# Kernel optimization log

Measured on AMD Instinct MI355X. Metric: run time of the kernel, lower is better.

The kernel has to match this reference:

```python
import jax, jax.numpy as jnp
import numpy as np

B, D, H = 256, 512, 256
K = 5
MARGIN = 1.0
TAU = 1.0
LAM_C = 0.01
LAM_E = 0.1
BETA = 0.1
LN_EPS = 1e-5


def _layernorm(x, g, b):
    mu = jnp.mean(x, axis=-1, keepdims=True)
    var = jnp.var(x, axis=-1, keepdims=True)
    return (x - mu) * jax.lax.rsqrt(var + LN_EPS) * g + b


def setup_inputs() -> dict:
    key = jax.random.key(0)
    ks = jax.random.split(key, 16)
    s = 0.02
    inp = {
        "outputs": jax.random.normal(ks[0], (B, 3, 64, 64), jnp.float32),
        "images": jax.random.normal(ks[1], (B, 3, 64, 64), jnp.float32),
        "f_orig": jax.random.normal(ks[2], (B, D), jnp.float32),
        "f_recon": jax.random.normal(ks[3], (B, D), jnp.float32),
        "cf1": jax.random.normal(ks[4], (B, 256, 8, 8), jnp.float32),
        "cf2": jax.random.normal(ks[5], (B, 512, 4, 4), jnp.float32),
        # EnergyNet encoder params
        "W1": jax.random.normal(ks[6], (D, H), jnp.float32) * s,
        "b1": jnp.zeros((H,), jnp.float32),
        "g1": jnp.ones((H,), jnp.float32),
        "be1": jnp.zeros((H,), jnp.float32),
        "W2": jax.random.normal(ks[7], (H, H), jnp.float32) * s,
        "b2": jnp.zeros((H,), jnp.float32),
        # EnergyNet interaction params
        "W3": jax.random.normal(ks[8], (3 * H, H), jnp.float32) * s,
        "b3": jnp.zeros((H,), jnp.float32),
        "g3": jnp.ones((H,), jnp.float32),
        "be3": jnp.zeros((H,), jnp.float32),
        "W4": jax.random.normal(ks[9], (H, H // 2), jnp.float32) * s,
        "b4": jnp.zeros((H // 2,), jnp.float32),
        "W5": jax.random.normal(ks[10], (H // 2, 1), jnp.float32) * s,
        "b5": jnp.zeros((1,), jnp.float32),
    }
    return inp


def _encoder(x, W1, b1, g1, be1, W2, b2):
    h = _layernorm(x @ W1 + b1, g1, be1)
    return jax.nn.relu(h) @ W2 + b2


def _energy_matrix(f1, f2, W1, b1, g1, be1, W2, b2, W3, b3, g3, be3, W4, b4, W5, b5):
    e1 = _encoder(f1, W1, b1, g1, be1, W2, b2)  # [B,H]
    e2 = _encoder(f2, W1, b1, g1, be1, W2, b2)  # [B,H]
    e1b = jnp.broadcast_to(e1[:, None, :], (B, B, H))
    e2b = jnp.broadcast_to(e2[None, :, :], (B, B, H))
    combined = jnp.concatenate([e1b, e2b, e1b * e2b], axis=-1)  # [B,B,3H]
    h = jax.nn.relu(_layernorm(combined @ W3 + b3, g3, be3))
    h = jax.nn.relu(h @ W4 + b4)
    return (h @ W5 + b5)[..., 0]  # [B,B]


def _topk_neighbors(f, k):
    fn = f / (jnp.linalg.norm(f, axis=1, keepdims=True))
    sim = fn @ fn.T
    sim = jnp.where(jnp.eye(f.shape[0], dtype=bool), -jnp.inf, sim)
    _, idx = jax.lax.top_k(sim, k)  # [B,k]
    onehot = jnp.zeros((f.shape[0], f.shape[0]), jnp.float32)
    rows = jnp.arange(f.shape[0])[:, None]
    return onehot.at[rows, idx].set(1.0)


def _entropy(x):
    xn = (x - x.min()) / (x.max() - x.min() + 1e-8)
    # torch.histc(bins=256, min=0, max=1): values at max go to last bin
    idx = jnp.clip(jnp.floor(xn.reshape(-1) * 256.0).astype(jnp.int32), 0, 255)
    hist = jnp.bincount(idx, length=256).astype(jnp.float32)
    p = hist / hist.sum()
    return -jnp.sum(p * jnp.log2(p + 1e-8))


def reference(outputs, images, f_orig, f_recon, cf1, cf2,
              W1, b1, g1, be1, W2, b2, W3, b3, g3, be3, W4, b4, W5, b5):
    # reconstruction loss
    recon = jnp.mean((outputs - images) ** 2)

    # energy margin loss
    E = _energy_matrix(f_orig, f_recon, W1, b1, g1, be1, W2, b2,
                       W3, b3, g3, be3, W4, b4, W5, b5)
    pos = jnp.diag(E)[:, None]
    losses = jax.nn.relu(MARGIN + E - pos)
    neg_mask = ~jnp.eye(B, dtype=bool)
    standard_loss = jnp.sum(losses * neg_mask) / (B * (B - 1))

    k = min(K, B - 1)
    on = _topk_neighbors(f_orig, k)
    rn = _topk_neighbors(f_recon, k)
    inter = jnp.sum(on * rn, axis=1)
    union = jnp.sum(jnp.clip(on + rn, 0.0, 1.0), axis=1)
    jaccard = inter / (union + 1e-8)
    neighbor_loss = 1.0 - jnp.mean(jaccard)
    energy_loss = standard_loss + 0.3 * neighbor_loss

    # compression loss over the dict of compressed features {cf1, cf2}
    sp = 0.5 * (jnp.mean(jnp.abs(cf1)) + jnp.mean(jnp.abs(cf2)))
    en = 0.5 * (_entropy(cf1) + _entropy(cf2))
    compress = sp + BETA * en

    total = recon + LAM_C * compress + LAM_E * energy_loss
    return (total, recon, energy_loss, compress)
```

## Files before the change

### kernel.cpp

```cpp
#include <hip/hip_runtime.h>
#include <math.h>

typedef __attribute__((ext_vector_type(8))) short short8;
typedef __attribute__((ext_vector_type(4))) float f32x4;


__device__ __forceinline__ float wave_sum(float v) {
#pragma unroll
    for (int o = 32; o > 0; o >>= 1) v += __shfl_down(v, o);
    return v;
}

__device__ __forceinline__ float block_sum256(float v, float* red) {
    v = wave_sum(v);
    int t = threadIdx.x;
    if ((t & 63) == 0) red[t >> 6] = v;
    __syncthreads();
    float r = red[0] + red[1] + red[2] + red[3];
    __syncthreads();
    return r;
}

__device__ __forceinline__ unsigned fenc(float f) {
    unsigned u = __float_as_uint(f);
    return (u & 0x80000000u) ? ~u : (u | 0x80000000u);
}
__device__ __forceinline__ float fdec(unsigned u) {
    return (u & 0x80000000u) ? __uint_as_float(u & 0x7fffffffu) : __uint_as_float(~u);
}

__device__ __forceinline__ ushort f2bf(float f) {
    unsigned u = __float_as_uint(f);
    unsigned r = (u + 0x7fffu + ((u >> 16) & 1u)) >> 16;
    return (ushort)r;
}


__global__ void init_kernel(float* wsf, unsigned* wsu, int* wsi) {
    int t = threadIdx.x;
    if (t < 7) wsf[t] = 0.f;
    if (t == 7 || t == 9) wsu[t] = 0xFFFFFFFFu;
    if (t == 8 || t == 10) wsu[t] = 0u;
    wsi[16 + t] = 0;
    wsi[272 + t] = 0;
}

__global__ __launch_bounds__(256) void stats_kernel(
    const float4* __restrict__ o, const float4* __restrict__ im,
    const float4* __restrict__ cf1, const float4* __restrict__ cf2,
    const float4* __restrict__ fo, const float4* __restrict__ fr,
    float* wsf, unsigned* wsu, float* rnorm) {
    __shared__ float red[4];
    __shared__ float rmn[4], rmx[4];
    int b = blockIdx.x, t = threadIdx.x;
    if (b < 512) {
        float s = 0.f;
        for (int i = b * 256 + t; i < 786432; i += 512 * 256) {
            float4 a = o[i], c = im[i];
            float dx = a.x - c.x, dy = a.y - c.y, dz = a.z - c.z, dw = a.w - c.w;
            s += dx * dx + dy * dy + dz * dz + dw * dw;
        }
        float tot = block_sum256(s, red);
        if (t == 0) atomicAdd(wsf + 0, tot);
    } else if (b < 1536) {
        int which = (b < 1024) ? 0 : 1;
        const float4* x = which ? cf2 : cf1;
        int n4 = which ? 524288 : 1048576;
        int b0 = which ? 1024 : 512;
        float s = 0.f, mn = INFINITY, mx = -INFINITY;
        for (int i = (b - b0) * 256 + t; i < n4; i += 512 * 256) {
            float4 a = x[i];
            s += fabsf(a.x) + fabsf(a.y) + fabsf(a.z) + fabsf(a.w);
            mn = fminf(mn, fminf(fminf(a.x, a.y), fminf(a.z, a.w)));
            mx = fmaxf(mx, fmaxf(fmaxf(a.x, a.y), fmaxf(a.z, a.w)));
        }
        float tot = block_sum256(s, red);
#pragma unroll
        for (int off = 32; off > 0; off >>= 1) {
            mn = fminf(mn, __shfl_down(mn, off));
            mx = fmaxf(mx, __shfl_down(mx, off));
        }
        if ((t & 63) == 0) { rmn[t >> 6] = mn; rmx[t >> 6] = mx; }
        __syncthreads();
        if (t == 0) {
            atomicAdd(wsf + 1 + which, tot);
            float m1 = fminf(fminf(rmn[0], rmn[1]), fminf(rmn[2], rmn[3]));
            float m2 = fmaxf(fmaxf(rmx[0], rmx[1]), fmaxf(rmx[2], rmx[3]));
            atomicMin(wsu + 7 + which * 2, fenc(m1));
            atomicMax(wsu + 8 + which * 2, fenc(m2));
        }
    } else {
        int r = b - 1536;
        const float4* f = (r < 256) ? (fo + (size_t)r * 128) : (fr + (size_t)(r - 256) * 128);
        float s = 0.f;
        if (t < 128) {
            float4 a = f[t];
            s = a.x * a.x + a.y * a.y + a.z * a.z + a.w * a.w;
        }
        float tot = block_sum256(s, red);
        if (t == 0) rnorm[r] = 1.0f / sqrtf(tot);
    }
}

__global__ __launch_bounds__(256) void hist_kernel(const float4* __restrict__ cf1,
                                                   const float4* __restrict__ cf2,
                                                   const unsigned* wsu, int* wsi) {
    __shared__ int hl[256];
    int b = blockIdx.x, t = threadIdx.x;
    hl[t] = 0;
    __syncthreads();
    int which = (b < 512) ? 0 : 1;
    const float4* x = which ? cf2 : cf1;
    int n4 = which ? 524288 : 1048576;
    int b0 = which ? 512 : 0;
    int* hist = wsi + (which ? 272 : 16);
    float mn = fdec(wsu[7 + which * 2]), mx = fdec(wsu[8 + which * 2]);
    float inv = 256.f / (mx - mn + 1e-8f);
    for (int i = (b - b0) * 256 + t; i < n4; i += 512 * 256) {
        float4 a = x[i];
        int b0i = min(max((int)floorf((a.x - mn) * inv), 0), 255);
        int b1i = min(max((int)floorf((a.y - mn) * inv), 0), 255);
        int b2i = min(max((int)floorf((a.z - mn) * inv), 0), 255);
        int b3i = min(max((int)floorf((a.w - mn) * inv), 0), 255);
        atomicAdd(&hl[b0i], 1);
        atomicAdd(&hl[b1i], 1);
        atomicAdd(&hl[b2i], 1);
        atomicAdd(&hl[b3i], 1);
    }
    __syncthreads();
    if (hl[t]) atomicAdd(&hist[t], hl[t]);
}

__global__ __launch_bounds__(256) void transpose_kernel(const float* __restrict__ fo,
                                                        const float* __restrict__ fr,
                                                        const float* __restrict__ rnorm,
                                                        float* __restrict__ fnT) {
    int b = blockIdx.x;
    int pass = b >> 6;
    int kt = (b >> 2) & 15;
    int jt = b & 3;
    int k0 = kt * 32, j0 = jt * 64;
    const float* f = pass ? fr : fo;
    const float* rn = rnorm + pass * 256;
    __shared__ float tile[64][33];
    int t = threadIdx.x;
    int cl = t & 31, rl = t >> 5;
#pragma unroll
    for (int r = 0; r < 8; ++r) {
        int row = j0 + rl + r * 8;
        tile[rl + r * 8][cl] = f[(size_t)row * 512 + k0 + cl] * rn[row];
    }
    __syncthreads();
    int jl = t & 63, kq = t >> 6;
    float* dst = fnT + (size_t)pass * 131072;
#pragma unroll
    for (int c = 0; c < 8; ++c) {
        int kl = kq * 8 + c;
        dst[(size_t)(k0 + kl) * 256 + j0 + jl] = tile[jl][kl];
    }
}

__global__ __launch_bounds__(256) void simtop_kernel(const float* __restrict__ fo,
                                                     const float* __restrict__ fr,
                                                     const float* __restrict__ rnorm,
                                                     const float* __restrict__ fnT,
                                                     int* __restrict__ top5) {
    int b = blockIdx.x;
    int pass = b >> 7, pair = b & 127;
    int i0 = pair * 2, i1 = i0 + 1;
    const float* f = pass ? fr : fo;
    const float* rn = rnorm + pass * 256;
    __shared__ float2 fs2[512];
    __shared__ float candV[4][2][5];
    __shared__ int candI[4][2][5];
    int t = threadIdx.x;
    float rn0 = rn[i0], rn1 = rn[i1];
    const float* f0 = f + (size_t)i0 * 512;
    const float* f1 = f + (size_t)i1 * 512;
    fs2[t] = make_float2(f0[t] * rn0, f1[t] * rn1);
    fs2[t + 256] = make_float2(f0[t + 256] * rn0, f1[t + 256] * rn1);
    __syncthreads();
    int j = t;
    const float* col = fnT + (size_t)pass * 131072 + j;
    float a0 = 0.f, a1 = 0.f;
#pragma unroll 16
    for (int k = 0; k < 512; ++k) {
        float v = col[(size_t)k * 256];
        float2 fv = fs2[k];
        a0 += fv.x * v;
        a1 += fv.y * v;
    }
    if (j == i0) a0 = -INFINITY;
    if (j == i1) a1 = -INFINITY;
    int w = t >> 6, lane = t & 63;
    for (int sel = 0; sel < 2; ++sel) {
        float v2 = sel ? a1 : a0;
        int idx = j;
        for (int r = 0; r < 5; ++r) {
            float m = v2;
            int mi = idx;
#pragma unroll
            for (int off = 32; off > 0; off >>= 1) {
                float om = __shfl_xor(m, off);
                int omi = __shfl_xor(mi, off);
                if (om > m || (om == m && omi < mi)) { m = om; mi = omi; }
            }
            if (lane == 0) { candV[w][sel][r] = m; candI[w][sel][r] = mi; }
            if (idx == mi) v2 = -INFINITY;
        }
    }
    __syncthreads();
    if (w < 2) {
        float v = -INFINITY;
        int ix = 0x7fffffff;
        if (lane < 20) { v = candV[lane / 5][w][lane % 5]; ix = candI[lane / 5][w][lane % 5]; }
        int iSel = w ? i1 : i0;
        for (int r = 0; r < 5; ++r) {
            float m = v;
            int mi = ix;
#pragma unroll
            for (int off = 32; off > 0; off >>= 1) {
                float om = __shfl_xor(m, off);
                int omi = __shfl_xor(mi, off);
                if (om > m || (om == m && omi < mi)) { m = om; mi = omi; }
            }
            if (lane == 0) top5[((size_t)pass * 256 + iSel) * 5 + r] = mi;
            if (ix == mi) v = -INFINITY;
        }
    }
}

__global__ void jaccard_kernel(const int* __restrict__ top5, float* jacOut) {
    __shared__ float red[4];
    int i = threadIdx.x;
    int O[5], R[5];
#pragma unroll
    for (int r = 0; r < 5; ++r) {
        O[r] = top5[i * 5 + r];
        R[r] = top5[(256 + i) * 5 + r];
    }
    int inter = 0;
#pragma unroll
    for (int a = 0; a < 5; ++a)
#pragma unroll
        for (int bq = 0; bq < 5; ++bq) inter += (O[a] == R[bq]);
    float fi2 = (float)inter;
    float jac = fi2 / (10.f - fi2 + 1e-8f);
    float s = block_sum256(jac, red);
    if (i == 0) jacOut[0] = s;
}

__global__ void encoder_kernel(const float* __restrict__ f_orig, const float* __restrict__ f_recon,
                               const float* __restrict__ W1, const float* __restrict__ b1,
                               const float* __restrict__ g1, const float* __restrict__ be1,
                               const float* __restrict__ W2, const float* __restrict__ b2,
                               const float* __restrict__ W3,
                               float* __restrict__ eAll, float* __restrict__ Aall) {
    int r = blockIdx.x;
    int t = threadIdx.x;
    const float* f = (r < 256) ? (f_orig + (size_t)r * 512) : (f_recon + (size_t)(r - 256) * 512);
    const float* W3p = (r < 256) ? W3 : (W3 + 256 * 256);
    __shared__ float fs[512];
    __shared__ float hs[256];
    __shared__ float es[256];
    __shared__ float red[4];
    fs[t] = f[t];
    fs[t + 256] = f[t + 256];
    __syncthreads();
    float x = b1[t];
    for (int k = 0; k < 512; ++k) x += fs[k] * W1[k * 256 + t];
    float s1 = block_sum256(x, red);
    float s2 = block_sum256(x * x, red);
    float mean = s1 * (1.f / 256.f);
    float var = s2 * (1.f / 256.f) - mean * mean;
    float rstd = rsqrtf(var + 1e-5f);
    float hn = (x - mean) * rstd * g1[t] + be1[t];
    hs[t] = fmaxf(hn, 0.f);
    __syncthreads();
    float e = b2[t];
    for (int k = 0; k < 256; ++k) e += hs[k] * W2[k * 256 + t];
    eAll[(size_t)r * 256 + t] = e;
    es[t] = e;
    __syncthreads();
    float a = 0.f;
    for (int k = 0; k < 256; ++k) a += es[k] * W3p[k * 256 + t];
    Aall[(size_t)r * 256 + t] = a;
}

__global__ void pack_kernel(const float* __restrict__ W3c, const float* __restrict__ W4,
                            ushort* __restrict__ W3p, ushort* __restrict__ W4p) {
    int b = blockIdx.x, t = threadIdx.x;
    if (b < 32) {
        int s = b * 256 + t;
        int lane = s & 63;
        int tt = (s >> 6) & 15;
        int kk = s >> 10;
        int qq = lane >> 4, nn = lane & 15;
        int tcol = tt * 16 + nn;
        short8 v;
#pragma unroll
        for (int jj = 0; jj < 8; ++jj) {
            int k = kk * 32 + qq * 8 + jj;
            v[jj] = (short)f2bf(W3c[(size_t)k * 256 + tcol]);
        }
        *(short8*)(W3p + (size_t)s * 8) = v;
    } else {
        int s = (b - 32) * 256 + t;
        int lane = s & 63;
        int tt = (s >> 6) & 7;
        int kk = s >> 9;
        int qq = lane >> 4, nn = lane & 15;
        int ncol = tt * 16 + nn;
        short8 v;
#pragma unroll
        for (int jj = 0; jj < 8; ++jj) {
            int k = kk * 32 + qq * 8 + jj;
            v[jj] = (short)f2bf(W4[(size_t)k * 128 + ncol]);
        }
        *(short8*)(W4p + (size_t)s * 8) = v;
    }
}

__global__ __launch_bounds__(256) void energy_mfma_kernel(
    const float* __restrict__ eAll, const float* __restrict__ Aall,
    const ushort* __restrict__ W3p, const ushort* __restrict__ W4p,
    const float* __restrict__ b3, const float* __restrict__ g3, const float* __restrict__ be3,
    const float* __restrict__ b4, const float* __restrict__ W5, const float* __restrict__ b5,
    float* __restrict__ E)
{
    int i = blockIdx.x >> 2;
    int jq = blockIdx.x & 3;
    int t = threadIdx.x;
    int w = t >> 6;
    int lane = t & 63;
    int q = lane >> 4;
    int n = lane & 15;
    int jbase = jq * 64 + w * 16;

    __shared__ float comb[256], g3s[256], be3s[256];
    __shared__ uint4 Bst[1024];
    __shared__ __align__(16) ushort Hs[4][16 * 264];

    const float* e1 = eAll + (size_t)i * 256;
    const float* e2 = eAll + 65536;
    const float* A1 = Aall + (size_t)i * 256;
    const float* A2 = Aall + 65536;

    comb[t] = A1[t] + b3[t];
    g3s[t] = g3[t];
    be3s[t] = be3[t];

    f32x4 acc[16];
#pragma unroll
    for (int x = 0; x < 16; ++x) acc[x] = (f32x4){0.f, 0.f, 0.f, 0.f};

    const float* e2row = e2 + (size_t)(jbase + n) * 256;

    for (int kk = 0; kk < 8; ++kk) {
        __syncthreads();
        {
            const uint4* src = (const uint4*)(W3p + (size_t)kk * 8192);
#pragma unroll
            for (int x = 0; x < 4; ++x) Bst[t * 4 + x] = src[t * 4 + x];
        }
        int kb = kk * 32 + q * 8;
        float4 ea0 = *(const float4*)(e2row + kb);
        float4 ea1 = *(const float4*)(e2row + kb + 4);
        float4 eb0 = *(const float4*)(e1 + kb);
        float4 eb1 = *(const float4*)(e1 + kb + 4);
        short8 af;
        af[0] = (short)f2bf(ea0.x * eb0.x);
        af[1] = (short)f2bf(ea0.y * eb0.y);
        af[2] = (short)f2bf(ea0.z * eb0.z);
        af[3] = (short)f2bf(ea0.w * eb0.w);
        af[4] = (short)f2bf(ea1.x * eb1.x);
        af[5] = (short)f2bf(ea1.y * eb1.y);
        af[6] = (short)f2bf(ea1.z * eb1.z);
        af[7] = (short)f2bf(ea1.w * eb1.w);
        __syncthreads();
        const short8* bst = (const short8*)Bst;
#pragma unroll
        for (int tt = 0; tt < 16; ++tt) {
            short8 bfr = bst[tt * 64 + lane];
            acc[tt] = __builtin_amdgcn_mfma_f32_16x16x32_bf16(af, bfr, acc[tt], 0, 0, 0);
        }
    }

    float s1[4] = {0.f, 0.f, 0.f, 0.f}, s2[4] = {0.f, 0.f, 0.f, 0.f};
#pragma unroll
    for (int tt = 0; tt < 16; ++tt) {
        int col = tt * 16 + n;
        float cb = comb[col];
#pragma unroll
        for (int r = 0; r < 4; ++r) {
            int jr = jbase + q * 4 + r;
            float v = acc[tt][r] + cb + A2[(size_t)jr * 256 + col];
            acc[tt][r] = v;
            s1[r] += v;
            s2[r] += v * v;
        }
    }
#pragma unroll
    for (int off = 1; off < 16; off <<= 1) {
#pragma unroll
        for (int r = 0; r < 4; ++r) {
            s1[r] += __shfl_xor(s1[r], off);
            s2[r] += __shfl_xor(s2[r], off);
        }
    }
    float mean[4], rstd[4];
#pragma unroll
    for (int r = 0; r < 4; ++r) {
        mean[r] = s1[r] * (1.f / 256.f);
        float var = s2[r] * (1.f / 256.f) - mean[r] * mean[r];
        rstd[r] = rsqrtf(var + 1e-5f);
    }
    ushort* hrow = Hs[w];
#pragma unroll
    for (int tt = 0; tt < 16; ++tt) {
        int col = tt * 16 + n;
        float gg = g3s[col], be = be3s[col];
#pragma unroll
        for (int r = 0; r < 4; ++r) {
            float hv = fmaxf((acc[tt][r] - mean[r]) * rstd[r] * gg + be, 0.f);
            hrow[(q * 4 + r) * 264 + col] = f2bf(hv);
        }
    }

    f32x4 gacc[8];
#pragma unroll
    for (int x = 0; x < 8; ++x) gacc[x] = (f32x4){0.f, 0.f, 0.f, 0.f};

    for (int kk = 0; kk < 8; ++kk) {
        __syncthreads();
        {
            const uint4* src = (const uint4*)(W4p + (size_t)kk * 4096);
#pragma unroll
            for (int x = 0; x < 2; ++x) Bst[t * 2 + x] = src[t * 2 + x];
        }
        short8 af = *(const short8*)(hrow + n * 264 + kk * 32 + q * 8);
        __syncthreads();
        const short8* bst = (const short8*)Bst;
#pragma unroll
        for (int tt = 0; tt < 8; ++tt) {
            short8 bfr = bst[tt * 64 + lane];
            gacc[tt] = __builtin_amdgcn_mfma_f32_16x16x32_bf16(af, bfr, gacc[tt], 0, 0, 0);
        }
    }

    float ep[4] = {0.f, 0.f, 0.f, 0.f};
    float b5v = b5[0];
#pragma unroll
    for (int tt = 0; tt < 8; ++tt) {
        int col = tt * 16 + n;
        float b4v = b4[col], w5v = W5[col];
#pragma unroll
        for (int r = 0; r < 4; ++r)
            ep[r] += fmaxf(gacc[tt][r] + b4v, 0.f) * w5v;
    }
#pragma unroll
    for (int off = 1; off < 16; off <<= 1) {
#pragma unroll
        for (int r = 0; r < 4; ++r) ep[r] += __shfl_xor(ep[r], off);
    }
    if (n == 0) {
#pragma unroll
        for (int r = 0; r < 4; ++r)
            E[(size_t)i * 256 + jbase + q * 4 + r] = ep[r] + b5v;
    }
}

__global__ void margin_kernel(const float* __restrict__ E, float* slAcc) {
    __shared__ float red[4];
    int i = blockIdx.x, t = threadIdx.x;
    float diag = E[(size_t)i * 256 + i];
    float l = (t == i) ? 0.f : fmaxf(1.f + E[(size_t)i * 256 + t] - diag, 0.f);
    float tot = block_sum256(l, red);
    if (t == 0) atomicAdd(slAcc, tot);
}

__global__ void finalize_kernel(const float* wsf, const int* h1, const int* h2, float* out) {
    __shared__ float red[4];
    int t = threadIdx.x;
    float p1 = (float)h1[t] / 4194304.f;
    float p2 = (float)h2[t] / 2097152.f;
    float s1 = block_sum256(-p1 * log2f(p1 + 1e-8f), red);
    float s2 = block_sum256(-p2 * log2f(p2 + 1e-8f), red);
    if (t == 0) {
        float recon = wsf[0] / 3145728.f;
        float sp = 0.5f * (wsf[1] / 4194304.f + wsf[2] / 2097152.f);
        float en = 0.5f * (s1 + s2);
        float compress = sp + 0.1f * en;
        float sl = wsf[5] / (256.f * 255.f);
        float nl = 1.f - wsf[6] / 256.f;
        float energy = sl + 0.3f * nl;
        float total = recon + 0.01f * compress + 0.1f * energy;
        out[0] = total;
        out[1] = recon;
        out[2] = energy;
        out[3] = compress;
    }
}

extern "C" void kernel_launch(void* const* d_in, const int* in_sizes, int n_in,
                              void* d_out, int out_size, void* d_ws, size_t ws_size,
                              hipStream_t stream) {
    const float* outputs = (const float*)d_in[0];
    const float* images  = (const float*)d_in[1];
    const float* f_orig  = (const float*)d_in[2];
    const float* f_recon = (const float*)d_in[3];
    const float* cf1 = (const float*)d_in[4];
    const float* cf2 = (const float*)d_in[5];
    const float* W1 = (const float*)d_in[6];
    const float* b1 = (const float*)d_in[7];
    const float* g1 = (const float*)d_in[8];
    const float* be1 = (const float*)d_in[9];
    const float* W2 = (const float*)d_in[10];
    const float* b2 = (const float*)d_in[11];
    const float* W3 = (const float*)d_in[12];
    const float* b3 = (const float*)d_in[13];
    const float* g3 = (const float*)d_in[14];
    const float* be3 = (const float*)d_in[15];
    const float* W4 = (const float*)d_in[16];
    const float* b4 = (const float*)d_in[17];
    const float* W5 = (const float*)d_in[18];
    const float* b5 = (const float*)d_in[19];

    float* wsf = (float*)d_ws;
    unsigned* wsu = (unsigned*)d_ws;
    int* wsi = (int*)d_ws;
    float* out = (float*)d_out;

    float* rnorm = wsf + 528;
    float* eAll = wsf + 1040;
    float* Aall = wsf + 132112;
    float* Emat = wsf + 263184;
    ushort* W3pk = (ushort*)(wsf + 328720);
    ushort* W4pk = (ushort*)(wsf + 361488);
    float* fnT = wsf + 377872;
    int* top5 = wsi + 640016;

    hipLaunchKernelGGL(init_kernel, dim3(1), dim3(256), 0, stream, wsf, wsu, wsi);
    hipLaunchKernelGGL(pack_kernel, dim3(48), dim3(256), 0, stream,
                       W3 + 512 * 256, W4, W3pk, W4pk);
    hipLaunchKernelGGL(stats_kernel, dim3(2048), dim3(256), 0, stream,
                       (const float4*)outputs, (const float4*)images,
                       (const float4*)cf1, (const float4*)cf2,
                       (const float4*)f_orig, (const float4*)f_recon,
                       wsf, wsu, rnorm);
    hipLaunchKernelGGL(hist_kernel, dim3(1024), dim3(256), 0, stream,
                       (const float4*)cf1, (const float4*)cf2, wsu, wsi);
    hipLaunchKernelGGL(transpose_kernel, dim3(128), dim3(256), 0, stream,
                       f_orig, f_recon, rnorm, fnT);
    hipLaunchKernelGGL(encoder_kernel, dim3(512), dim3(256), 0, stream,
                       f_orig, f_recon, W1, b1, g1, be1, W2, b2, W3, eAll, Aall);
    hipLaunchKernelGGL(simtop_kernel, dim3(256), dim3(256), 0, stream,
                       f_orig, f_recon, rnorm, fnT, top5);
    hipLaunchKernelGGL(energy_mfma_kernel, dim3(1024), dim3(256), 0, stream,
                       eAll, Aall, W3pk, W4pk, b3, g3, be3, b4, W5, b5, Emat);
    hipLaunchKernelGGL(margin_kernel, dim3(256), dim3(256), 0, stream, Emat, wsf + 5);
    hipLaunchKernelGGL(jaccard_kernel, dim3(1), dim3(256), 0, stream, top5, wsf + 6);
    hipLaunchKernelGGL(finalize_kernel, dim3(1), dim3(256), 0, stream,
                       wsf, wsi + 16, wsi + 272, out);
}
```

Measured before the change: 278.2 us.

## Fuse prologue kernels into one launch and restructure energy MFMA kernel

Merges the stats, transpose, weight-pack and encoder kernels into one multi-role kernel dispatched by block index, and merges the margin and jaccard kernels. This cuts the number of launches and the serialization between small kernels. The energy kernel is rewritten so each block handles a whole row i, with bf16 intermediates and register shuffles replacing the shared-memory staging of the hidden layer. Cosine normalisation now happens after the dot product, which removes the dependency of the transpose on rnorm. The single-block-per-CU launch bound and the larger register tiles risk lower occupancy.

```diff
diff --git a/kernel.cpp b/kernel.cpp
--- a/kernel.cpp
+++ b/kernel.cpp
@@ -3,6 +3,9 @@
 
 typedef __attribute__((ext_vector_type(8))) short short8;
 typedef __attribute__((ext_vector_type(4))) float f32x4;
+typedef __attribute__((ext_vector_type(4))) unsigned int u32x4;
+
+union U8 { unsigned int u[4]; short8 s; u32x4 v; };
 
 
 __device__ __forceinline__ float wave_sum(float v) {
@@ -34,6 +37,8 @@
     unsigned r = (u + 0x7fffu + ((u >> 16) & 1u)) >> 16;
     return (ushort)r;
 }
+__device__ __forceinline__ float bflo(unsigned u) { return __uint_as_float(u << 16); }
+__device__ __forceinline__ float bfhi(unsigned u) { return __uint_as_float(u & 0xffff0000u); }
 
 
 __global__ void init_kernel(float* wsf, unsigned* wsu, int* wsi) {
@@ -45,60 +50,155 @@
     wsi[272 + t] = 0;
 }
 
-__global__ __launch_bounds__(256) void stats_kernel(
+__global__ __launch_bounds__(256) void mega_kernel(
     const float4* __restrict__ o, const float4* __restrict__ im,
     const float4* __restrict__ cf1, const float4* __restrict__ cf2,
-    const float4* __restrict__ fo, const float4* __restrict__ fr,
-    float* wsf, unsigned* wsu, float* rnorm) {
-    __shared__ float red[4];
-    __shared__ float rmn[4], rmx[4];
+    const float* __restrict__ fo, const float* __restrict__ fr,
+    const float* __restrict__ W1, const float* __restrict__ b1,
+    const float* __restrict__ g1, const float* __restrict__ be1,
+    const float* __restrict__ W2, const float* __restrict__ b2,
+    const float* __restrict__ W3,
+    float* wsf, unsigned* wsu, float* rnorm, float* fT,
+    float* __restrict__ A1, ushort* __restrict__ A2bf, ushort* __restrict__ ebf,
+    ushort* __restrict__ W3pk, ushort* __restrict__ W4pk, const float* __restrict__ W4) {
+    __shared__ float smem[64 * 33];
+    float* red = smem;
     int b = blockIdx.x, t = threadIdx.x;
-    if (b < 512) {
-        float s = 0.f;
-        for (int i = b * 256 + t; i < 786432; i += 512 * 256) {
-            float4 a = o[i], c = im[i];
-            float dx = a.x - c.x, dy = a.y - c.y, dz = a.z - c.z, dw = a.w - c.w;
-            s += dx * dx + dy * dy + dz * dz + dw * dw;
-        }
-        float tot = block_sum256(s, red);
-        if (t == 0) atomicAdd(wsf + 0, tot);
-    } else if (b < 1536) {
-        int which = (b < 1024) ? 0 : 1;
-        const float4* x = which ? cf2 : cf1;
-        int n4 = which ? 524288 : 1048576;
-        int b0 = which ? 1024 : 512;
-        float s = 0.f, mn = INFINITY, mx = -INFINITY;
-        for (int i = (b - b0) * 256 + t; i < n4; i += 512 * 256) {
-            float4 a = x[i];
-            s += fabsf(a.x) + fabsf(a.y) + fabsf(a.z) + fabsf(a.w);
-            mn = fminf(mn, fminf(fminf(a.x, a.y), fminf(a.z, a.w)));
-            mx = fmaxf(mx, fmaxf(fmaxf(a.x, a.y), fmaxf(a.z, a.w)));
-        }
-        float tot = block_sum256(s, red);
-#pragma unroll
-        for (int off = 32; off > 0; off >>= 1) {
-            mn = fminf(mn, __shfl_down(mn, off));
-            mx = fmaxf(mx, __shfl_down(mx, off));
-        }
-        if ((t & 63) == 0) { rmn[t >> 6] = mn; rmx[t >> 6] = mx; }
+    if (b < 2048) {
+        if (b < 512) {
+            float s = 0.f;
+            for (int i = b * 256 + t; i < 786432; i += 512 * 256) {
+                float4 a = o[i], c = im[i];
+                float dx = a.x - c.x, dy = a.y - c.y, dz = a.z - c.z, dw = a.w - c.w;
+                s += dx * dx + dy * dy + dz * dz + dw * dw;
+            }
+            float tot = block_sum256(s, red);
+            if (t == 0) atomicAdd(wsf + 0, tot);
+        } else if (b < 1536) {
+            int which = (b < 1024) ? 0 : 1;
+            const float4* x = which ? cf2 : cf1;
+            int n4 = which ? 524288 : 1048576;
+            int b0 = which ? 1024 : 512;
+            float s = 0.f, mn = INFINITY, mx = -INFINITY;
+            for (int i = (b - b0) * 256 + t; i < n4; i += 512 * 256) {
+                float4 a = x[i];
+                s += fabsf(a.x) + fabsf(a.y) + fabsf(a.z) + fabsf(a.w);
+                mn = fminf(mn, fminf(fminf(a.x, a.y), fminf(a.z, a.w)));
+                mx = fmaxf(mx, fmaxf(fmaxf(a.x, a.y), fmaxf(a.z, a.w)));
+            }
+            float tot = block_sum256(s, red);
+#pragma unroll
+            for (int off = 32; off > 0; off >>= 1) {
+                mn = fminf(mn, __shfl_down(mn, off));
+                mx = fmaxf(mx, __shfl_down(mx, off));
+            }
+            float* rmn = smem + 8;
+            float* rmx = smem + 16;
+            if ((t & 63) == 0) { rmn[t >> 6] = mn; rmx[t >> 6] = mx; }
+            __syncthreads();
+            if (t == 0) {
+                atomicAdd(wsf + 1 + which, tot);
+                float m1 = fminf(fminf(rmn[0], rmn[1]), fminf(rmn[2], rmn[3]));
+                float m2 = fmaxf(fmaxf(rmx[0], rmx[1]), fmaxf(rmx[2], rmx[3]));
+                atomicMin(wsu + 7 + which * 2, fenc(m1));
+                atomicMax(wsu + 8 + which * 2, fenc(m2));
+            }
+        } else {
+            int r = b - 1536;
+            const float4* f = (r < 256) ? ((const float4*)fo + (size_t)r * 128)
+                                        : ((const float4*)fr + (size_t)(r - 256) * 128);
+            float s = 0.f;
+            if (t < 128) {
+                float4 a = f[t];
+                s = a.x * a.x + a.y * a.y + a.z * a.z + a.w * a.w;
+            }
+            float tot = block_sum256(s, red);
+            if (t == 0) rnorm[r] = 1.0f / sqrtf(tot);
+        }
+    } else if (b < 2176) {
+        int bb = b - 2048;
+        int pass = bb >> 6;
+        int kt = (bb >> 2) & 15;
+        int jt = bb & 3;
+        int k0 = kt * 32, j0 = jt * 64;
+        const float* f = pass ? fr : fo;
+        float (*tile)[33] = (float(*)[33])smem;
+        int cl = t & 31, rl = t >> 5;
+#pragma unroll
+        for (int r = 0; r < 8; ++r) {
+            int row = j0 + rl + r * 8;
+            tile[rl + r * 8][cl] = f[(size_t)row * 512 + k0 + cl];
+        }
         __syncthreads();
-        if (t == 0) {
-            atomicAdd(wsf + 1 + which, tot);
-            float m1 = fminf(fminf(rmn[0], rmn[1]), fminf(rmn[2], rmn[3]));
-            float m2 = fmaxf(fmaxf(rmx[0], rmx[1]), fmaxf(rmx[2], rmx[3]));
-            atomicMin(wsu + 7 + which * 2, fenc(m1));
-            atomicMax(wsu + 8 + which * 2, fenc(m2));
+        int jl = t & 63, kq = t >> 6;
+        float* dst = fT + (size_t)pass * 131072;
+#pragma unroll
+        for (int c = 0; c < 8; ++c) {
+            int kl = kq * 8 + c;
+            dst[(size_t)(k0 + kl) * 256 + j0 + jl] = tile[jl][kl];
+        }
+    } else if (b < 2224) {
+        int pb = b - 2176;
+        const float* W3c = W3 + 512 * 256;
+        if (pb < 32) {
+            int s = pb * 256 + t;
+            int lane = s & 63;
+            int tt = (s >> 6) & 15;
+            int kk = s >> 10;
+            int qq = lane >> 4, nn = lane & 15;
+            int tcol = tt * 16 + nn;
+            short8 v;
+#pragma unroll
+            for (int jj = 0; jj < 8; ++jj) {
+                int k = kk * 32 + qq * 8 + jj;
+                v[jj] = (short)f2bf(W3c[(size_t)k * 256 + tcol]);
+            }
+            *(short8*)(W3pk + (size_t)s * 8) = v;
+        } else {
+            int s = (pb - 32) * 256 + t;
+            int lane = s & 63;
+            int tt = (s >> 6) & 7;
+            int kk = s >> 9;
+            int qq = lane >> 4, nn = lane & 15;
+            int ncol = tt * 16 + nn;
+            short8 v;
+#pragma unroll
+            for (int jj = 0; jj < 8; ++jj) {
+                int k = kk * 32 + qq * 8 + jj;
+                v[jj] = (short)f2bf(W4[(size_t)k * 128 + ncol]);
+            }
+            *(short8*)(W4pk + (size_t)s * 8) = v;
         }
     } else {
-        int r = b - 1536;
-        const float4* f = (r < 256) ? (fo + (size_t)r * 128) : (fr + (size_t)(r - 256) * 128);
-        float s = 0.f;
-        if (t < 128) {
-            float4 a = f[t];
-            s = a.x * a.x + a.y * a.y + a.z * a.z + a.w * a.w;
-        }
-        float tot = block_sum256(s, red);
-        if (t == 0) rnorm[r] = 1.0f / sqrtf(tot);
+        int r = b - 2224;
+        const float* f = (r < 256) ? (fo + (size_t)r * 512) : (fr + (size_t)(r - 256) * 512);
+        const float* W3p = (r < 256) ? W3 : (W3 + 256 * 256);
+        float* fs = smem;
+        float* hs = smem + 512;
+        float* es = smem + 768;
+        float* rd = smem + 1024;
+        fs[t] = f[t];
+        fs[t + 256] = f[t + 256];
+        __syncthreads();
+        float x = b1[t];
+        for (int k = 0; k < 512; ++k) x += fs[k] * W1[k * 256 + t];
+        float s1 = block_sum256(x, rd);
+        float s2 = block_sum256(x * x, rd);
+        float mean = s1 * (1.f / 256.f);
+        float var = s2 * (1.f / 256.f) - mean * mean;
+        float rstd = rsqrtf(var + 1e-5f);
+        float hn = (x - mean) * rstd * g1[t] + be1[t];
+        hs[t] = fmaxf(hn, 0.f);
+        __syncthreads();
+        float e = b2[t];
+        for (int k = 0; k < 256; ++k) e += hs[k] * W2[k * 256 + t];
+        ebf[(size_t)r * 256 + t] = f2bf(e);
+        es[t] = e;
+        __syncthreads();
+        float a = 0.f;
+        for (int k = 0; k < 256; ++k) a += es[k] * W3p[k * 256 + t];
+        if (r < 256) A1[(size_t)r * 256 + t] = a;
+        else A2bf[(size_t)(r - 256) * 256 + t] = f2bf(a);
     }
 }
 
@@ -131,39 +231,10 @@
     if (hl[t]) atomicAdd(&hist[t], hl[t]);
 }
 
-__global__ __launch_bounds__(256) void transpose_kernel(const float* __restrict__ fo,
-                                                        const float* __restrict__ fr,
-                                                        const float* __restrict__ rnorm,
-                                                        float* __restrict__ fnT) {
-    int b = blockIdx.x;
-    int pass = b >> 6;
-    int kt = (b >> 2) & 15;
-    int jt = b & 3;
-    int k0 = kt * 32, j0 = jt * 64;
-    const float* f = pass ? fr : fo;
-    const float* rn = rnorm + pass * 256;
-    __shared__ float tile[64][33];
-    int t = threadIdx.x;
-    int cl = t & 31, rl = t >> 5;
-#pragma unroll
-    for (int r = 0; r < 8; ++r) {
-        int row = j0 + rl + r * 8;
-        tile[rl + r * 8][cl] = f[(size_t)row * 512 + k0 + cl] * rn[row];
-    }
-    __syncthreads();
-    int jl = t & 63, kq = t >> 6;
-    float* dst = fnT + (size_t)pass * 131072;
-#pragma unroll
-    for (int c = 0; c < 8; ++c) {
-        int kl = kq * 8 + c;
-        dst[(size_t)(k0 + kl) * 256 + j0 + jl] = tile[jl][kl];
-    }
-}
-
 __global__ __launch_bounds__(256) void simtop_kernel(const float* __restrict__ fo,
                                                      const float* __restrict__ fr,
                                                      const float* __restrict__ rnorm,
-                                                     const float* __restrict__ fnT,
+                                                     const float* __restrict__ fT,
                                                      int* __restrict__ top5) {
     int b = blockIdx.x;
     int pass = b >> 7, pair = b & 127;
@@ -174,14 +245,13 @@
     __shared__ float candV[4][2][5];
     __shared__ int candI[4][2][5];
     int t = threadIdx.x;
-    float rn0 = rn[i0], rn1 = rn[i1];
     const float* f0 = f + (size_t)i0 * 512;
     const float* f1 = f + (size_t)i1 * 512;
-    fs2[t] = make_float2(f0[t] * rn0, f1[t] * rn1);
-    fs2[t + 256] = make_float2(f0[t + 256] * rn0, f1[t + 256] * rn1);
+    fs2[t] = make_float2(f0[t], f1[t]);
+    fs2[t + 256] = make_float2(f0[t + 256], f1[t + 256]);
     __syncthreads();
     int j = t;
-    const float* col = fnT + (size_t)pass * 131072 + j;
+    const float* col = fT + (size_t)pass * 131072 + j;
     float a0 = 0.f, a1 = 0.f;
 #pragma unroll 16
     for (int k = 0; k < 512; ++k) {
@@ -190,6 +260,9 @@
         a0 += fv.x * v;
         a1 += fv.y * v;
     }
+    float rnj = rn[j];
+    a0 *= rnj;
+    a1 *= rnj;
     if (j == i0) a0 = -INFINITY;
     if (j == i1) a1 = -INFINITY;
     int w = t >> 6, lane = t & 63;
@@ -230,253 +303,189 @@
     }
 }
 
-__global__ void jaccard_kernel(const int* __restrict__ top5, float* jacOut) {
-    __shared__ float red[4];
-    int i = threadIdx.x;
-    int O[5], R[5];
-#pragma unroll
-    for (int r = 0; r < 5; ++r) {
-        O[r] = top5[i * 5 + r];
-        R[r] = top5[(256 + i) * 5 + r];
-    }
-    int inter = 0;
-#pragma unroll
-    for (int a = 0; a < 5; ++a)
-#pragma unroll
-        for (int bq = 0; bq < 5; ++bq) inter += (O[a] == R[bq]);
-    float fi2 = (float)inter;
-    float jac = fi2 / (10.f - fi2 + 1e-8f);
-    float s = block_sum256(jac, red);
-    if (i == 0) jacOut[0] = s;
-}
-
-__global__ void encoder_kernel(const float* __restrict__ f_orig, const float* __restrict__ f_recon,
-                               const float* __restrict__ W1, const float* __restrict__ b1,
-                               const float* __restrict__ g1, const float* __restrict__ be1,
-                               const float* __restrict__ W2, const float* __restrict__ b2,
-                               const float* __restrict__ W3,
-                               float* __restrict__ eAll, float* __restrict__ Aall) {
-    int r = blockIdx.x;
-    int t = threadIdx.x;
-    const float* f = (r < 256) ? (f_orig + (size_t)r * 512) : (f_recon + (size_t)(r - 256) * 512);
-    const float* W3p = (r < 256) ? W3 : (W3 + 256 * 256);
-    __shared__ float fs[512];
-    __shared__ float hs[256];
-    __shared__ float es[256];
-    __shared__ float red[4];
-    fs[t] = f[t];
-    fs[t + 256] = f[t + 256];
-    __syncthreads();
-    float x = b1[t];
-    for (int k = 0; k < 512; ++k) x += fs[k] * W1[k * 256 + t];
-    float s1 = block_sum256(x, red);
-    float s2 = block_sum256(x * x, red);
-    float mean = s1 * (1.f / 256.f);
-    float var = s2 * (1.f / 256.f) - mean * mean;
-    float rstd = rsqrtf(var + 1e-5f);
-    float hn = (x - mean) * rstd * g1[t] + be1[t];
-    hs[t] = fmaxf(hn, 0.f);
-    __syncthreads();
-    float e = b2[t];
-    for (int k = 0; k < 256; ++k) e += hs[k] * W2[k * 256 + t];
-    eAll[(size_t)r * 256 + t] = e;
-    es[t] = e;
-    __syncthreads();
-    float a = 0.f;
-    for (int k = 0; k < 256; ++k) a += es[k] * W3p[k * 256 + t];
-    Aall[(size_t)r * 256 + t] = a;
-}
-
-__global__ void pack_kernel(const float* __restrict__ W3c, const float* __restrict__ W4,
-                            ushort* __restrict__ W3p, ushort* __restrict__ W4p) {
-    int b = blockIdx.x, t = threadIdx.x;
-    if (b < 32) {
-        int s = b * 256 + t;
-        int lane = s & 63;
-        int tt = (s >> 6) & 15;
-        int kk = s >> 10;
-        int qq = lane >> 4, nn = lane & 15;
-        int tcol = tt * 16 + nn;
-        short8 v;
-#pragma unroll
-        for (int jj = 0; jj < 8; ++jj) {
-            int k = kk * 32 + qq * 8 + jj;
-            v[jj] = (short)f2bf(W3c[(size_t)k * 256 + tcol]);
-        }
-        *(short8*)(W3p + (size_t)s * 8) = v;
-    } else {
-        int s = (b - 32) * 256 + t;
-        int lane = s & 63;
-        int tt = (s >> 6) & 7;
-        int kk = s >> 9;
-        int qq = lane >> 4, nn = lane & 15;
-        int ncol = tt * 16 + nn;
-        short8 v;
-#pragma unroll
-        for (int jj = 0; jj < 8; ++jj) {
-            int k = kk * 32 + qq * 8 + jj;
-            v[jj] = (short)f2bf(W4[(size_t)k * 128 + ncol]);
-        }
-        *(short8*)(W4p + (size_t)s * 8) = v;
-    }
-}
-
-__global__ __launch_bounds__(256) void energy_mfma_kernel(
-    const float* __restrict__ eAll, const float* __restrict__ Aall,
+__global__ __launch_bounds__(256, 1) void energy_v3(
+    const float* __restrict__ A1, const ushort* __restrict__ A2bf,
+    const ushort* __restrict__ ebf,
     const ushort* __restrict__ W3p, const ushort* __restrict__ W4p,
     const float* __restrict__ b3, const float* __restrict__ g3, const float* __restrict__ be3,
     const float* __restrict__ b4, const float* __restrict__ W5, const float* __restrict__ b5,
     float* __restrict__ E)
 {
-    int i = blockIdx.x >> 2;
-    int jq = blockIdx.x & 3;
+    int i = blockIdx.x;
     int t = threadIdx.x;
-    int w = t >> 6;
-    int lane = t & 63;
-    int q = lane >> 4;
-    int n = lane & 15;
-    int jbase = jq * 64 + w * 16;
-
-    __shared__ float comb[256], g3s[256], be3s[256];
-    __shared__ uint4 Bst[1024];
-    __shared__ __align__(16) ushort Hs[4][16 * 264];
-
-    const float* e1 = eAll + (size_t)i * 256;
-    const float* e2 = eAll + 65536;
-    const float* A1 = Aall + (size_t)i * 256;
-    const float* A2 = Aall + 65536;
-
-    comb[t] = A1[t] + b3[t];
-    g3s[t] = g3[t];
-    be3s[t] = be3[t];
-
-    f32x4 acc[16];
-#pragma unroll
-    for (int x = 0; x < 16; ++x) acc[x] = (f32x4){0.f, 0.f, 0.f, 0.f};
-
-    const float* e2row = e2 + (size_t)(jbase + n) * 256;
+    int w = t >> 6, lane = t & 63, q = lane >> 4, n = lane & 15;
+    int jb = w * 64;
+    __shared__ float combS[256], g3S[256], be3S[256], b4S[128], w5S[128];
+    combS[t] = A1[(size_t)i * 256 + t] + b3[t];
+    g3S[t] = g3[t];
+    be3S[t] = be3[t];
+    if (t < 128) { b4S[t] = b4[t]; w5S[t] = W5[t]; }
+    __syncthreads();
+
+    const ushort* e1p = ebf + (size_t)i * 256;
+    const ushort* e2p = ebf + 65536;
+
+    f32x4 acc[4][16];
+#pragma unroll
+    for (int s = 0; s < 4; ++s)
+#pragma unroll
+        for (int tt = 0; tt < 16; ++tt) acc[s][tt] = (f32x4){0.f, 0.f, 0.f, 0.f};
 
     for (int kk = 0; kk < 8; ++kk) {
-        __syncthreads();
-        {
-            const uint4* src = (const uint4*)(W3p + (size_t)kk * 8192);
-#pragma unroll
-            for (int x = 0; x < 4; ++x) Bst[t * 4 + x] = src[t * 4 + x];
-        }
-        int kb = kk * 32 + q * 8;
-        float4 ea0 = *(const float4*)(e2row + kb);
-        float4 ea1 = *(const float4*)(e2row + kb + 4);
-        float4 eb0 = *(const float4*)(e1 + kb);
-        float4 eb1 = *(const float4*)(e1 + kb + 4);
-        short8 af;
-        af[0] = (short)f2bf(ea0.x * eb0.x);
-        af[1] = (short)f2bf(ea0.y * eb0.y);
-        af[2] = (short)f2bf(ea0.z * eb0.z);
-        af[3] = (short)f2bf(ea0.w * eb0.w);
-        af[4] = (short)f2bf(ea1.x * eb1.x);
-        af[5] = (short)f2bf(ea1.y * eb1.y);
-        af[6] = (short)f2bf(ea1.z * eb1.z);
-        af[7] = (short)f2bf(ea1.w * eb1.w);
-        __syncthreads();
-        const short8* bst = (const short8*)Bst;
+        int kbase = kk * 32 + q * 8;
+        U8 e1v;
+        e1v.v = *(const u32x4*)(e1p + kbase);
+        float e1f[8];
+#pragma unroll
+        for (int x = 0; x < 4; ++x) {
+            e1f[2 * x] = bflo(e1v.u[x]);
+            e1f[2 * x + 1] = bfhi(e1v.u[x]);
+        }
+        short8 bfrag[4];
+#pragma unroll
+        for (int s = 0; s < 4; ++s) {
+            U8 e2v;
+            e2v.v = *(const u32x4*)(e2p + (size_t)(jb + s * 16 + n) * 256 + kbase);
+            U8 bb;
+#pragma unroll
+            for (int x = 0; x < 4; ++x) {
+                float p0 = bflo(e2v.u[x]) * e1f[2 * x];
+                float p1 = bfhi(e2v.u[x]) * e1f[2 * x + 1];
+                bb.u[x] = (unsigned)f2bf(p0) | ((unsigned)f2bf(p1) << 16);
+            }
+            bfrag[s] = bb.s;
+        }
+        const ushort* wp = W3p + ((size_t)(kk * 16) * 64 + lane) * 8;
 #pragma unroll
         for (int tt = 0; tt < 16; ++tt) {
-            short8 bfr = bst[tt * 64 + lane];
-            acc[tt] = __builtin_amdgcn_mfma_f32_16x16x32_bf16(af, bfr, acc[tt], 0, 0, 0);
-        }
-    }
-
-    float s1[4] = {0.f, 0.f, 0.f, 0.f}, s2[4] = {0.f, 0.f, 0.f, 0.f};
-#pragma unroll
-    for (int tt = 0; tt < 16; ++tt) {
-        int col = tt * 16 + n;
-        float cb = comb[col];
-#pragma unroll
-        for (int r = 0; r < 4; ++r) {
-            int jr = jbase + q * 4 + r;
-            float v = acc[tt][r] + cb + A2[(size_t)jr * 256 + col];
-            acc[tt][r] = v;
-            s1[r] += v;
-            s2[r] += v * v;
-        }
-    }
-#pragma unroll
-    for (int off = 1; off < 16; off <<= 1) {
-#pragma unroll
-        for (int r = 0; r < 4; ++r) {
-            s1[r] += __shfl_xor(s1[r], off);
-            s2[r] += __shfl_xor(s2[r], off);
-        }
-    }
-    float mean[4], rstd[4];
-#pragma unroll
-    for (int r = 0; r < 4; ++r) {
-        mean[r] = s1[r] * (1.f / 256.f);
-        float var = s2[r] * (1.f / 256.f) - mean[r] * mean[r];
-        rstd[r] = rsqrtf(var + 1e-5f);
-    }
-    ushort* hrow = Hs[w];
-#pragma unroll
-    for (int tt = 0; tt < 16; ++tt) {
-        int col = tt * 16 + n;
-        float gg = g3s[col], be = be3s[col];
-#pragma unroll
-        for (int r = 0; r < 4; ++r) {
-            float hv = fmaxf((acc[tt][r] - mean[r]) * rstd[r] * gg + be, 0.f);
-            hrow[(q * 4 + r) * 264 + col] = f2bf(hv);
-        }
-    }
-
-    f32x4 gacc[8];
-#pragma unroll
-    for (int x = 0; x < 8; ++x) gacc[x] = (f32x4){0.f, 0.f, 0.f, 0.f};
-
+            short8 af = *(const short8*)(wp + (size_t)tt * 512);
+#pragma unroll
+            for (int s = 0; s < 4; ++s)
+                acc[s][tt] = __builtin_amdgcn_mfma_f32_16x16x32_bf16(af, bfrag[s], acc[s][tt], 0, 0, 0);
+        }
+    }
+
+    uint2 pk[4][16];
+    float b5v = b5[0];
+#pragma unroll
+    for (int s = 0; s < 4; ++s) {
+        int j = jb + s * 16 + n;
+        float s1 = 0.f, s2 = 0.f;
+#pragma unroll
+        for (int tt = 0; tt < 16; ++tt) {
+            int tb = tt * 16 + q * 4;
+            float4 cb = *(const float4*)(combS + tb);
+            uint2 a2u = *(const uint2*)(A2bf + (size_t)j * 256 + tb);
+            float a0 = bflo(a2u.x), a1f = bfhi(a2u.x), a2f = bflo(a2u.y), a3f = bfhi(a2u.y);
+            float v0 = acc[s][tt][0] + cb.x + a0;
+            float v1 = acc[s][tt][1] + cb.y + a1f;
+            float v2 = acc[s][tt][2] + cb.z + a2f;
+            float v3 = acc[s][tt][3] + cb.w + a3f;
+            acc[s][tt][0] = v0; acc[s][tt][1] = v1; acc[s][tt][2] = v2; acc[s][tt][3] = v3;
+            s1 += v0 + v1 + v2 + v3;
+            s2 += v0 * v0 + v1 * v1 + v2 * v2 + v3 * v3;
+        }
+        s1 += __shfl_xor(s1, 16); s1 += __shfl_xor(s1, 32);
+        s2 += __shfl_xor(s2, 16); s2 += __shfl_xor(s2, 32);
+        float mean = s1 * (1.f / 256.f);
+        float var = s2 * (1.f / 256.f) - mean * mean;
+        float rstd = rsqrtf(var + 1e-5f);
+#pragma unroll
+        for (int tt = 0; tt < 16; ++tt) {
+            int tb = tt * 16 + q * 4;
+            float4 gg = *(const float4*)(g3S + tb);
+            float4 be = *(const float4*)(be3S + tb);
+            float h0 = fmaxf((acc[s][tt][0] - mean) * rstd * gg.x + be.x, 0.f);
+            float h1 = fmaxf((acc[s][tt][1] - mean) * rstd * gg.y + be.y, 0.f);
+            float h2 = fmaxf((acc[s][tt][2] - mean) * rstd * gg.z + be.z, 0.f);
+            float h3 = fmaxf((acc[s][tt][3] - mean) * rstd * gg.w + be.w, 0.f);
+            pk[s][tt].x = (unsigned)f2bf(h0) | ((unsigned)f2bf(h1) << 16);
+            pk[s][tt].y = (unsigned)f2bf(h2) | ((unsigned)f2bf(h3) << 16);
+        }
+    }
+
+    f32x4 gacc[4][8];
+#pragma unroll
+    for (int s = 0; s < 4; ++s)
+#pragma unroll
+        for (int nt = 0; nt < 8; ++nt) gacc[s][nt] = (f32x4){0.f, 0.f, 0.f, 0.f};
+
+    int qh = (q >> 1) & 1;
+    int src0 = ((q & 1) * 2) * 16 + n;
+    int src1 = src0 + 16;
+#pragma unroll
     for (int kk = 0; kk < 8; ++kk) {
-        __syncthreads();
-        {
-            const uint4* src = (const uint4*)(W4p + (size_t)kk * 4096);
-#pragma unroll
-            for (int x = 0; x < 2; ++x) Bst[t * 2 + x] = src[t * 2 + x];
-        }
-        short8 af = *(const short8*)(hrow + n * 264 + kk * 32 + q * 8);
-        __syncthreads();
-        const short8* bst = (const short8*)Bst;
-#pragma unroll
-        for (int tt = 0; tt < 8; ++tt) {
-            short8 bfr = bst[tt * 64 + lane];
-            gacc[tt] = __builtin_amdgcn_mfma_f32_16x16x32_bf16(af, bfr, gacc[tt], 0, 0, 0);
-        }
-    }
-
-    float ep[4] = {0.f, 0.f, 0.f, 0.f};
-    float b5v = b5[0];
-#pragma unroll
-    for (int tt = 0; tt < 8; ++tt) {
-        int col = tt * 16 + n;
-        float b4v = b4[col], w5v = W5[col];
-#pragma unroll
-        for (int r = 0; r < 4; ++r)
-            ep[r] += fmaxf(gacc[tt][r] + b4v, 0.f) * w5v;
-    }
-#pragma unroll
-    for (int off = 1; off < 16; off <<= 1) {
-#pragma unroll
-        for (int r = 0; r < 4; ++r) ep[r] += __shfl_xor(ep[r], off);
-    }
-    if (n == 0) {
-#pragma unroll
-        for (int r = 0; r < 4; ++r)
-            E[(size_t)i * 256 + jbase + q * 4 + r] = ep[r] + b5v;
-    }
-}
-
-__global__ void margin_kernel(const float* __restrict__ E, float* slAcc) {
+        short8 wa[8];
+        const ushort* wp = W4p + ((size_t)(kk * 8) * 64 + lane) * 8;
+#pragma unroll
+        for (int nt = 0; nt < 8; ++nt) wa[nt] = *(const short8*)(wp + (size_t)nt * 512);
+#pragma unroll
+        for (int s = 0; s < 4; ++s) {
+            uint2 lo2 = pk[s][kk * 2], hi2 = pk[s][kk * 2 + 1];
+            unsigned a0 = (unsigned)__shfl((int)lo2.x, src0);
+            unsigned a1 = (unsigned)__shfl((int)lo2.y, src0);
+            unsigned b0 = (unsigned)__shfl((int)hi2.x, src0);
+            unsigned b1 = (unsigned)__shfl((int)hi2.y, src0);
+            unsigned c0 = (unsigned)__shfl((int)lo2.x, src1);
+            unsigned c1 = (unsigned)__shfl((int)lo2.y, src1);
+            unsigned d0 = (unsigned)__shfl((int)hi2.x, src1);
+            unsigned d1 = (unsigned)__shfl((int)hi2.y, src1);
+            U8 hb;
+            hb.u[0] = qh ? b0 : a0;
+            hb.u[1] = qh ? b1 : a1;
+            hb.u[2] = qh ? d0 : c0;
+            hb.u[3] = qh ? d1 : c1;
+#pragma unroll
+            for (int nt = 0; nt < 8; ++nt)
+                gacc[s][nt] = __builtin_amdgcn_mfma_f32_16x16x32_bf16(wa[nt], hb.s, gacc[s][nt], 0, 0, 0);
+        }
+    }
+
+#pragma unroll
+    for (int s = 0; s < 4; ++s) {
+        float ep = 0.f;
+#pragma unroll
+        for (int nt = 0; nt < 8; ++nt) {
+            int nb = nt * 16 + q * 4;
+            float4 b4v = *(const float4*)(b4S + nb);
+            float4 w5v = *(const float4*)(w5S + nb);
+            ep += fmaxf(gacc[s][nt][0] + b4v.x, 0.f) * w5v.x;
+            ep += fmaxf(gacc[s][nt][1] + b4v.y, 0.f) * w5v.y;
+            ep += fmaxf(gacc[s][nt][2] + b4v.z, 0.f) * w5v.z;
+            ep += fmaxf(gacc[s][nt][3] + b4v.w, 0.f) * w5v.w;
+        }
+        ep += __shfl_xor(ep, 16);
+        ep += __shfl_xor(ep, 32);
+        if (q == 0) E[(size_t)i * 256 + jb + s * 16 + n] = ep + b5v;
+    }
+}
+
+__global__ void margin_jac_kernel(const float* __restrict__ E, const int* __restrict__ top5,
+                                  float* slAcc, float* jacOut) {
     __shared__ float red[4];
-    int i = blockIdx.x, t = threadIdx.x;
-    float diag = E[(size_t)i * 256 + i];
-    float l = (t == i) ? 0.f : fmaxf(1.f + E[(size_t)i * 256 + t] - diag, 0.f);
-    float tot = block_sum256(l, red);
-    if (t == 0) atomicAdd(slAcc, tot);
+    int b = blockIdx.x, t = threadIdx.x;
+    if (b < 256) {
+        float diag = E[(size_t)b * 256 + b];
+        float l = (t == b) ? 0.f : fmaxf(1.f + E[(size_t)b * 256 + t] - diag, 0.f);
+        float tot = block_sum256(l, red);
+        if (t == 0) atomicAdd(slAcc, tot);
+    } else {
+        int O[5], R[5];
+#pragma unroll
+        for (int r = 0; r < 5; ++r) {
+            O[r] = top5[t * 5 + r];
+            R[r] = top5[(256 + t) * 5 + r];
+        }
+        int inter = 0;
+#pragma unroll
+        for (int a = 0; a < 5; ++a)
+#pragma unroll
+            for (int bq = 0; bq < 5; ++bq) inter += (O[a] == R[bq]);
+        float fi2 = (float)inter;
+        float jac = fi2 / (10.f - fi2 + 1e-8f);
+        float s = block_sum256(jac, red);
+        if (t == 0) jacOut[0] = s;
+    }
 }
 
 __global__ void finalize_kernel(const float* wsf, const int* h1, const int* h2, float* out) {
@@ -532,34 +541,29 @@
     float* out = (float*)d_out;
 
     float* rnorm = wsf + 528;
-    float* eAll = wsf + 1040;
-    float* Aall = wsf + 132112;
-    float* Emat = wsf + 263184;
-    ushort* W3pk = (ushort*)(wsf + 328720);
-    ushort* W4pk = (ushort*)(wsf + 361488);
-    float* fnT = wsf + 377872;
-    int* top5 = wsi + 640016;
+    float* A1 = wsf + 1040;
+    ushort* A2bf = (ushort*)(wsf + 66576);
+    ushort* ebf = (ushort*)(wsf + 82960);
+    float* Emat = wsf + 148496;
+    ushort* W3pk = (ushort*)(wsf + 214032);
+    ushort* W4pk = (ushort*)(wsf + 230416);
+    float* fT = wsf + 238608;
+    int* top5 = wsi + 500752;
 
     hipLaunchKernelGGL(init_kernel, dim3(1), dim3(256), 0, stream, wsf, wsu, wsi);
-    hipLaunchKernelGGL(pack_kernel, dim3(48), dim3(256), 0, stream,
-                       W3 + 512 * 256, W4, W3pk, W4pk);
-    hipLaunchKernelGGL(stats_kernel, dim3(2048), dim3(256), 0, stream,
+    hipLaunchKernelGGL(mega_kernel, dim3(2736), dim3(256), 0, stream,
                        (const float4*)outputs, (const float4*)images,
                        (const float4*)cf1, (const float4*)cf2,
-                       (const float4*)f_orig, (const float4*)f_recon,
-                       wsf, wsu, rnorm);
+                       f_orig, f_recon, W1, b1, g1, be1, W2, b2, W3,
+                       wsf, wsu, rnorm, fT, A1, A2bf, ebf, W3pk, W4pk, W4);
     hipLaunchKernelGGL(hist_kernel, dim3(1024), dim3(256), 0, stream,
                        (const float4*)cf1, (const float4*)cf2, wsu, wsi);
-    hipLaunchKernelGGL(transpose_kernel, dim3(128), dim3(256), 0, stream,
-                       f_orig, f_recon, rnorm, fnT);
-    hipLaunchKernelGGL(encoder_kernel, dim3(512), dim3(256), 0, stream,
-                       f_orig, f_recon, W1, b1, g1, be1, W2, b2, W3, eAll, Aall);
     hipLaunchKernelGGL(simtop_kernel, dim3(256), dim3(256), 0, stream,
-                       f_orig, f_recon, rnorm, fnT, top5);
-    hipLaunchKernelGGL(energy_mfma_kernel, dim3(1024), dim3(256), 0, stream,
-                       eAll, Aall, W3pk, W4pk, b3, g3, be3, b4, W5, b5, Emat);
-    hipLaunchKernelGGL(margin_kernel, dim3(256), dim3(256), 0, stream, Emat, wsf + 5);
-    hipLaunchKernelGGL(jaccard_kernel, dim3(1), dim3(256), 0, stream, top5, wsf + 6);
+                       f_orig, f_recon, rnorm, fT, top5);
+    hipLaunchKernelGGL(energy_v3, dim3(256), dim3(256), 0, stream,
+                       A1, A2bf, ebf, W3pk, W4pk, b3, g3, be3, b4, W5, b5, Emat);
+    hipLaunchKernelGGL(margin_jac_kernel, dim3(257), dim3(256), 0, stream,
+                       Emat, top5, wsf + 5, wsf + 6);
     hipLaunchKernelGGL(finalize_kernel, dim3(1), dim3(256), 0, stream,
                        wsf, wsi + 16, wsi + 272, out);
 }
```

Result: no change. 283.2 us (+1.8%).
